# Optimization experiments

Hardware: AMD Instinct MI355X
Metric: run time of the kernel (lower is better)

The kernel has to match this reference:

```python
import jax, jax.numpy as jnp
import numpy as np

B, C, H, W = 8, 256, 64, 64
CK = C // 8  # query/key channels


def setup_inputs() -> dict:
    key = jax.random.key(0)
    ks = jax.random.split(key, 8)
    s = 1.0 / np.sqrt(C)
    return {
        "x": jax.random.normal(ks[0], (B, C, H, W), dtype=jnp.float32),
        "Wq": jax.random.normal(ks[1], (CK, C), dtype=jnp.float32) * s,
        "bq": jax.random.normal(ks[2], (CK,), dtype=jnp.float32) * 0.01,
        "Wk": jax.random.normal(ks[3], (CK, C), dtype=jnp.float32) * s,
        "bk": jax.random.normal(ks[4], (CK,), dtype=jnp.float32) * 0.01,
        "Wv": jax.random.normal(ks[5], (C, C), dtype=jnp.float32) * s,
        "bv": jax.random.normal(ks[6], (C,), dtype=jnp.float32) * 0.01,
        "gamma": jax.random.normal(ks[7], (1,), dtype=jnp.float32) * 0.1,
    }


def reference(x, Wq, bq, Wk, bk, Wv, bv, gamma):
    b, c, h, w = x.shape
    n = h * w
    xf = x.reshape(b, c, n)                       # [B,C,N]
    # 1x1 convs == channel-wise linear maps
    q = jnp.einsum('oc,bcn->bon', Wq, xf) + bq[:, None]   # [B,CK,N]
    k = jnp.einsum('oc,bcn->bon', Wk, xf) + bk[:, None]   # [B,CK,N]
    v = jnp.einsum('oc,bcn->bon', Wv, xf) + bv[:, None]   # [B,C,N]
    energy = jnp.einsum('bcm,bcn->bmn', q, k)             # [B,N,N] (query rows m)
    attn = jax.nn.softmax(energy, axis=-1)
    out = jnp.einsum('bcn,bmn->bcm', v, attn)             # value @ attn^T
    out = out.reshape(b, c, h, w)
    return gamma * out + x
```

## Files before the change

### kernel.cpp

```cpp
#include <hip/hip_runtime.h>
#include <stdint.h>

typedef unsigned short u16;
typedef __bf16 bf16_t;
typedef __bf16 bf16x4 __attribute__((ext_vector_type(4)));
typedef __bf16 bf16x8 __attribute__((ext_vector_type(8)));
typedef float f32x4 __attribute__((ext_vector_type(4)));

#define LOG2E 1.4426950408889634f

__device__ __forceinline__ u16 f2bf(float f) {
    union { float f; unsigned int u; } v; v.f = f;
    unsigned int r = v.u + 0x7fffu + ((v.u >> 16) & 1u);
    return (u16)(r >> 16);
}

__device__ __forceinline__ bf16x8 ld8f_bf(const float* __restrict__ p) {
    float4 a = *reinterpret_cast<const float4*>(p);
    float4 b = *reinterpret_cast<const float4*>(p + 4);
    bf16x8 r;
    r[0] = (bf16_t)a.x; r[1] = (bf16_t)a.y; r[2] = (bf16_t)a.z; r[3] = (bf16_t)a.w;
    r[4] = (bf16_t)b.x; r[5] = (bf16_t)b.y; r[6] = (bf16_t)b.z; r[7] = (bf16_t)b.w;
    return r;
}

__global__ __launch_bounds__(256) void k_transpose(const float* __restrict__ x,
                                                   u16* __restrict__ xT) {
    __shared__ u16 tile[64][68];
    int blk = blockIdx.x;
    int b = blk >> 8;
    int r = blk & 255;
    int c0 = (r & 3) * 64;
    int n0 = (r >> 2) * 64;
    const float* xb = x + (size_t)b * 256 * 4096;
    u16* xTb = xT + (size_t)b * 4096 * 256;
    int t = threadIdx.x;
    int lc = t >> 4;
    int l4 = (t & 15) * 4;
    #pragma unroll
    for (int p = 0; p < 4; ++p) {
        int c = lc + p * 16;
        float4 v = *reinterpret_cast<const float4*>(xb + (size_t)(c0 + c) * 4096 + n0 + l4);
        tile[c][l4 + 0] = f2bf(v.x); tile[c][l4 + 1] = f2bf(v.y);
        tile[c][l4 + 2] = f2bf(v.z); tile[c][l4 + 3] = f2bf(v.w);
    }
    __syncthreads();
    #pragma unroll
    for (int p = 0; p < 4; ++p) {
        int n = lc + p * 16;
        ushort4 v;
        v.x = tile[l4 + 0][n]; v.y = tile[l4 + 1][n];
        v.z = tile[l4 + 2][n]; v.w = tile[l4 + 3][n];
        *reinterpret_cast<ushort4*>(xTb + (size_t)(n0 + n) * 256 + c0 + l4) = v;
    }
}

__global__ __launch_bounds__(256, 2) void k_proj(
    const u16* __restrict__ xT,
    const float* __restrict__ Wq, const float* __restrict__ bq,
    const float* __restrict__ Wk, const float* __restrict__ bk,
    const float* __restrict__ Wv, const float* __restrict__ bv,
    u16* __restrict__ qt, u16* __restrict__ kt, u16* __restrict__ vn) {
    __shared__ u16 Xs[64 * 256];
    __shared__ u16 Ws[64 * 256];
    __shared__ u16 Wvs[256 * 32];
    int blk = blockIdx.x;
    int b = blk & 7;
    int n0 = (blk >> 3) * 64;
    int t = threadIdx.x;
    int w = t >> 6;
    int lane = t & 63;
    int lo = lane & 15;
    int q = lane >> 4;
    const u16* xTb = xT + (size_t)b * 4096 * 256;

    #pragma unroll
    for (int p = 0; p < 8; ++p) {
        int G = p * 256 + t;
        int n = G >> 5, g = G & 31;
        bf16x8 v = *reinterpret_cast<const bf16x8*>(
            xTb + (size_t)(n0 + n) * 256 + g * 8);
        *reinterpret_cast<bf16x8*>(&Xs[(n * 32 + (g ^ (n & 7))) * 8]) = v;
        const float* src = (n < 32) ? (Wq + (size_t)n * 256 + g * 8)
                                    : (Wk + (size_t)(n - 32) * 256 + g * 8);
        *reinterpret_cast<bf16x8*>(&Ws[(n * 32 + (g ^ (n & 7))) * 8]) = ld8f_bf(src);
    }

    f32x4 accqk[4] = {};
    f32x4 accv[16];
    #pragma unroll
    for (int i = 0; i < 16; ++i) accv[i] = f32x4{0.f, 0.f, 0.f, 0.f};

    int rowA = w * 16 + lo;
    int cw = w * 64;
    for (int c0 = 0; c0 < 256; c0 += 32) {
        __syncthreads();
        #pragma unroll
        for (int p = 0; p < 4; ++p) {
            int G = p * 256 + t;
            int co = G >> 2, g2 = G & 3;
            *reinterpret_cast<bf16x8*>(&Wvs[(co * 4 + (g2 ^ (co & 3))) * 8]) =
                ld8f_bf(Wv + (size_t)co * 256 + c0 + g2 * 8);
        }
        __syncthreads();

        int K = c0 >> 3;
        bf16x8 a = *reinterpret_cast<const bf16x8*>(
            &Xs[(rowA * 32 + ((K + q) ^ (lo & 7))) * 8]);
        #pragma unroll
        for (int ot = 0; ot < 4; ++ot) {
            bf16x8 bb = *reinterpret_cast<const bf16x8*>(
                &Ws[((ot * 16 + lo) * 32 + ((K + q) ^ (lo & 7))) * 8]);
            accqk[ot] = __builtin_amdgcn_mfma_f32_16x16x32_bf16(a, bb, accqk[ot], 0, 0, 0);
        }
        bf16x8 xbf[4];
        #pragma unroll
        for (int nt = 0; nt < 4; ++nt)
            xbf[nt] = *reinterpret_cast<const bf16x8*>(
                &Xs[((nt * 16 + lo) * 32 + ((K + q) ^ (lo & 7))) * 8]);
        #pragma unroll
        for (int ct = 0; ct < 4; ++ct) {
            int co = cw + ct * 16 + lo;
            bf16x8 av = *reinterpret_cast<const bf16x8*>(
                &Wvs[(co * 4 + (q ^ (co & 3))) * 8]);
            #pragma unroll
            for (int nt = 0; nt < 4; ++nt)
                accv[ct * 4 + nt] = __builtin_amdgcn_mfma_f32_16x16x32_bf16(
                    av, xbf[nt], accv[ct * 4 + nt], 0, 0, 0);
        }
    }
    #pragma unroll
    for (int ot = 0; ot < 4; ++ot) {
        float bias = (ot < 2) ? bq[ot * 16 + lo] : bk[(ot - 2) * 16 + lo];
        #pragma unroll
        for (int r = 0; r < 4; ++r) {
            int n = n0 + w * 16 + q * 4 + r;
            float val = accqk[ot][r] + bias;
            if (ot < 2) qt[((size_t)b * 4096 + n) * 32 + ot * 16 + lo] = f2bf(val);
            else        kt[((size_t)b * 4096 + n) * 32 + (ot - 2) * 16 + lo] = f2bf(val);
        }
    }
    #pragma unroll
    for (int ct = 0; ct < 4; ++ct) {
        #pragma unroll
        for (int nt = 0; nt < 4; ++nt) {
            #pragma unroll
            for (int r = 0; r < 4; ++r) {
                int co = cw + ct * 16 + q * 4 + r;
                float val = accv[ct * 4 + nt][r] + bv[co];
                vn[((size_t)b * 256 + co) * 4096 + n0 + nt * 16 + lo] = f2bf(val);
            }
        }
    }
}

__global__ __launch_bounds__(256, 2) void k_flash(
    const u16* __restrict__ qt, const u16* __restrict__ kt,
    const u16* __restrict__ vn, const float* __restrict__ x,
    const float* __restrict__ gamma, float* __restrict__ out) {
    __shared__ bf16_t E_lds[2][128 * 72];
    __shared__ float l_lds[128];
    int blk = blockIdx.x;
    int b = blk & 7;
    int rest = blk >> 3;
    int m0 = (rest & 31) * 128;
    int ch0 = (rest >> 5) * 128;
    int t = threadIdx.x;
    int w = t >> 6;
    int lane = t & 63;
    int lo = lane & 15;
    int q = lane >> 4;
    const u16* qtb = qt + (size_t)b * 4096 * 32;
    const u16* ktb = kt + (size_t)b * 4096 * 32;
    const u16* vb = vn + (size_t)b * 256 * 4096;

    int qw0 = m0 + w * 32;
    int cw0 = ch0 + w * 32;

    bf16x8 qfrag[2];
    #pragma unroll
    for (int qm = 0; qm < 2; ++qm)
        qfrag[qm] = *reinterpret_cast<const bf16x8*>(
            qtb + (size_t)(qw0 + qm * 16 + lo) * 32 + q * 8);

    f32x4 O[2][8];
    #pragma unroll
    for (int ct = 0; ct < 2; ++ct)
        #pragma unroll
        for (int mt = 0; mt < 8; ++mt) O[ct][mt] = f32x4{0.f, 0.f, 0.f, 0.f};
    float lsum[2] = {0.f, 0.f};
    const f32x4 zero = {0.f, 0.f, 0.f, 0.f};

    {
        bf16x8 kf[4];
        #pragma unroll
        for (int nt = 0; nt < 4; ++nt)
            kf[nt] = *reinterpret_cast<const bf16x8*>(
                ktb + (size_t)(nt * 16 + lo) * 32 + q * 8);
        #pragma unroll
        for (int qm = 0; qm < 2; ++qm)
            #pragma unroll
            for (int nt = 0; nt < 4; ++nt) {
                f32x4 St = __builtin_amdgcn_mfma_f32_16x16x32_bf16(
                    kf[nt], qfrag[qm], zero, 0, 0, 0);
                bf16x4 pp;
                #pragma unroll
                for (int r = 0; r < 4; ++r) {
                    float p = __builtin_amdgcn_exp2f(St[r] * LOG2E);
                    lsum[qm] += p;
                    pp[r] = (bf16_t)p;
                }
                *reinterpret_cast<bf16x4*>(
                    &E_lds[0][(qw0 - m0 + qm * 16 + lo) * 72 + nt * 16 + q * 4]) = pp;
            }
    }
    __syncthreads();

    for (int s = 0; s < 64; ++s) {
        int n0 = s * 64;
        const bf16_t* Er = E_lds[s & 1];
        bf16_t* Ew = E_lds[(s + 1) & 1];
        if (s + 1 < 64) {
            bf16x8 kf[4];
            #pragma unroll
            for (int nt = 0; nt < 4; ++nt)
                kf[nt] = *reinterpret_cast<const bf16x8*>(
                    ktb + (size_t)(n0 + 64 + nt * 16 + lo) * 32 + q * 8);
            #pragma unroll
            for (int qm = 0; qm < 2; ++qm)
                #pragma unroll
                for (int nt = 0; nt < 4; ++nt) {
                    f32x4 St = __builtin_amdgcn_mfma_f32_16x16x32_bf16(
                        kf[nt], qfrag[qm], zero, 0, 0, 0);
                    bf16x4 pp;
                    #pragma unroll
                    for (int r = 0; r < 4; ++r) {
                        float p = __builtin_amdgcn_exp2f(St[r] * LOG2E);
                        lsum[qm] += p;
                        pp[r] = (bf16_t)p;
                    }
                    *reinterpret_cast<bf16x4*>(
                        &Ew[(qw0 - m0 + qm * 16 + lo) * 72 + nt * 16 + q * 4]) = pp;
                }
        }
        #pragma unroll
        for (int kk = 0; kk < 2; ++kk) {
            bf16x8 vf[2];
            #pragma unroll
            for (int ct = 0; ct < 2; ++ct)
                vf[ct] = *reinterpret_cast<const bf16x8*>(
                    vb + (size_t)(cw0 + ct * 16 + lo) * 4096 + n0 + kk * 32 + q * 8);
            #pragma unroll
            for (int mt = 0; mt < 8; ++mt) {
                bf16x8 pf = *reinterpret_cast<const bf16x8*>(
                    &Er[(mt * 16 + lo) * 72 + kk * 32 + q * 8]);
                #pragma unroll
                for (int ct = 0; ct < 2; ++ct)
                    O[ct][mt] = __builtin_amdgcn_mfma_f32_16x16x32_bf16(
                        vf[ct], pf, O[ct][mt], 0, 0, 0);
            }
        }
        __syncthreads();
    }

    #pragma unroll
    for (int qm = 0; qm < 2; ++qm) {
        lsum[qm] += __shfl_xor(lsum[qm], 16, 64);
        lsum[qm] += __shfl_xor(lsum[qm], 32, 64);
        if (q == 0) l_lds[qw0 - m0 + qm * 16 + lo] = lsum[qm];
    }
    __syncthreads();

    float g = gamma[0];
    const float* xb = x + (size_t)b * 256 * 4096;
    float* ob = out + (size_t)b * 256 * 4096;
    float linv[8];
    #pragma unroll
    for (int mt = 0; mt < 8; ++mt) linv[mt] = 1.0f / l_lds[mt * 16 + lo];
    #pragma unroll
    for (int ct = 0; ct < 2; ++ct) {
        #pragma unroll
        for (int mt = 0; mt < 8; ++mt) {
            int m = m0 + mt * 16 + lo;
            #pragma unroll
            for (int r = 0; r < 4; ++r) {
                int c = cw0 + ct * 16 + q * 4 + r;
                size_t idx = (size_t)c * 4096 + m;
                ob[idx] = g * (O[ct][mt][r] * linv[mt]) + xb[idx];
            }
        }
    }
}

extern "C" void kernel_launch(void* const* d_in, const int* in_sizes, int n_in,
                              void* d_out, int out_size, void* d_ws, size_t ws_size,
                              hipStream_t stream) {
    const float* x     = (const float*)d_in[0];
    const float* Wq    = (const float*)d_in[1];
    const float* bq    = (const float*)d_in[2];
    const float* Wk    = (const float*)d_in[3];
    const float* bk    = (const float*)d_in[4];
    const float* Wv    = (const float*)d_in[5];
    const float* bv    = (const float*)d_in[6];
    const float* gamma = (const float*)d_in[7];
    float* out = (float*)d_out;

    char* ws = (char*)d_ws;
    u16* xT = (u16*)d_out;
    u16* qt = (u16*)ws;
    u16* kt = (u16*)(ws + 2097152);
    u16* vn = (u16*)(ws + 2 * 2097152);

    k_transpose<<<2048, 256, 0, stream>>>(x, xT);
    k_proj<<<512, 256, 0, stream>>>(xT, Wq, bq, Wk, bk, Wv, bv, qt, kt, vn);
    k_flash<<<512, 256, 0, stream>>>(qt, kt, vn, x, gamma, out);
}
```

Before: 237.9 us.

## Keep softmax probabilities in registers with 32x32 MFMA, dropping LDS staging

Measured after the change: 370.5 us. +55.8%, slower.

```diff
diff --git a/kernel.cpp b/kernel.cpp
--- a/kernel.cpp
+++ b/kernel.cpp
@@ -2,12 +2,15 @@
 #include <stdint.h>
 
 typedef unsigned short u16;
+typedef unsigned int u32;
 typedef __bf16 bf16_t;
 typedef __bf16 bf16x4 __attribute__((ext_vector_type(4)));
 typedef __bf16 bf16x8 __attribute__((ext_vector_type(8)));
 typedef float f32x4 __attribute__((ext_vector_type(4)));
+typedef float f32x16 __attribute__((ext_vector_type(16)));
 
 #define LOG2E 1.4426950408889634f
+#define MFMA32(a, b, c) __builtin_amdgcn_mfma_f32_32x32x16_bf16(a, b, c, 0, 0, 0)
 
 __device__ __forceinline__ u16 f2bf(float f) {
     union { float f; unsigned int u; } v; v.f = f;
@@ -22,6 +25,28 @@
     r[0] = (bf16_t)a.x; r[1] = (bf16_t)a.y; r[2] = (bf16_t)a.z; r[3] = (bf16_t)a.w;
     r[4] = (bf16_t)b.x; r[5] = (bf16_t)b.y; r[6] = (bf16_t)b.z; r[7] = (bf16_t)b.w;
     return r;
+}
+
+__device__ __forceinline__ u32 cvt_pk_bf16(float a, float b) {
+    u32 r;
+    asm("v_cvt_pk_bf16_f32 %0, %1, %2" : "=v"(r) : "v"(a), "v"(b));
+    return r;
+}
+
+__device__ __forceinline__ void plane32_swap(u32& a, u32& b) {
+    asm("v_permlane32_swap_b32 %0, %1" : "+v"(a), "+v"(b));
+}
+
+__device__ __forceinline__ bf16x8 pack8(const float* p) {
+    u32 c0 = cvt_pk_bf16(p[0], p[1]);
+    u32 c1 = cvt_pk_bf16(p[2], p[3]);
+    u32 c2 = cvt_pk_bf16(p[4], p[5]);
+    u32 c3 = cvt_pk_bf16(p[6], p[7]);
+    plane32_swap(c0, c2);
+    plane32_swap(c1, c3);
+    union { u32 u[4]; bf16x8 v; } f;
+    f.u[0] = c0; f.u[1] = c1; f.u[2] = c2; f.u[3] = c3;
+    return f.v;
 }
 
 __global__ __launch_bounds__(256) void k_transpose(const float* __restrict__ x,
@@ -136,7 +161,7 @@
         for (int r = 0; r < 4; ++r) {
             int n = n0 + w * 16 + q * 4 + r;
             float val = accqk[ot][r] + bias;
-            if (ot < 2) qt[((size_t)b * 4096 + n) * 32 + ot * 16 + lo] = f2bf(val);
+            if (ot < 2) qt[((size_t)b * 4096 + n) * 32 + ot * 16 + lo] = f2bf(val * LOG2E);
             else        kt[((size_t)b * 4096 + n) * 32 + (ot - 2) * 16 + lo] = f2bf(val);
         }
     }
@@ -158,8 +183,6 @@
     const u16* __restrict__ qt, const u16* __restrict__ kt,
     const u16* __restrict__ vn, const float* __restrict__ x,
     const float* __restrict__ gamma, float* __restrict__ out) {
-    __shared__ bf16_t E_lds[2][128 * 72];
-    __shared__ float l_lds[128];
     int blk = blockIdx.x;
     int b = blk & 7;
     int rest = blk >> 3;
@@ -168,127 +191,118 @@
     int t = threadIdx.x;
     int w = t >> 6;
     int lane = t & 63;
-    int lo = lane & 15;
-    int q = lane >> 4;
+    int la = lane & 31;
+    int hi = lane >> 5;
+
     const u16* qtb = qt + (size_t)b * 4096 * 32;
     const u16* ktb = kt + (size_t)b * 4096 * 32;
-    const u16* vb = vn + (size_t)b * 256 * 4096;
+    const u16* vbp = vn + (size_t)b * 256 * 4096;
 
     int qw0 = m0 + w * 32;
-    int cw0 = ch0 + w * 32;
-
-    bf16x8 qfrag[2];
-    #pragma unroll
-    for (int qm = 0; qm < 2; ++qm)
-        qfrag[qm] = *reinterpret_cast<const bf16x8*>(
-            qtb + (size_t)(qw0 + qm * 16 + lo) * 32 + q * 8);
-
-    f32x4 O[2][8];
-    #pragma unroll
-    for (int ct = 0; ct < 2; ++ct)
-        #pragma unroll
-        for (int mt = 0; mt < 8; ++mt) O[ct][mt] = f32x4{0.f, 0.f, 0.f, 0.f};
-    float lsum[2] = {0.f, 0.f};
-    const f32x4 zero = {0.f, 0.f, 0.f, 0.f};
-
-    {
-        bf16x8 kf[4];
-        #pragma unroll
-        for (int nt = 0; nt < 4; ++nt)
-            kf[nt] = *reinterpret_cast<const bf16x8*>(
-                ktb + (size_t)(nt * 16 + lo) * 32 + q * 8);
-        #pragma unroll
-        for (int qm = 0; qm < 2; ++qm)
-            #pragma unroll
-            for (int nt = 0; nt < 4; ++nt) {
-                f32x4 St = __builtin_amdgcn_mfma_f32_16x16x32_bf16(
-                    kf[nt], qfrag[qm], zero, 0, 0, 0);
-                bf16x4 pp;
-                #pragma unroll
-                for (int r = 0; r < 4; ++r) {
-                    float p = __builtin_amdgcn_exp2f(St[r] * LOG2E);
-                    lsum[qm] += p;
-                    pp[r] = (bf16_t)p;
-                }
-                *reinterpret_cast<bf16x4*>(
-                    &E_lds[0][(qw0 - m0 + qm * 16 + lo) * 72 + nt * 16 + q * 4]) = pp;
-            }
-    }
-    __syncthreads();
+    bf16x8 qf0 = *reinterpret_cast<const bf16x8*>(qtb + (size_t)(qw0 + la) * 32 + hi * 8);
+    bf16x8 qf1 = *reinterpret_cast<const bf16x8*>(qtb + (size_t)(qw0 + la) * 32 + 16 + hi * 8);
+
+    f32x16 O0 = {}, O1 = {}, O2 = {}, O3 = {};
+    const f32x16 z16 = {};
+    float lsum = 0.f;
+
+    const u16* kp  = ktb + (size_t)la * 32 + hi * 8;
+    const u16* vp0 = vbp + (size_t)(ch0 +  0 + la) * 4096 + hi * 8;
+    const u16* vp1 = vbp + (size_t)(ch0 + 32 + la) * 4096 + hi * 8;
+    const u16* vp2 = vbp + (size_t)(ch0 + 64 + la) * 4096 + hi * 8;
+    const u16* vp3 = vbp + (size_t)(ch0 + 96 + la) * 4096 + hi * 8;
+
+    bf16x8 kf0 = *reinterpret_cast<const bf16x8*>(kp);
+    bf16x8 kf1 = *reinterpret_cast<const bf16x8*>(kp + 16);
+    bf16x8 kf2 = *reinterpret_cast<const bf16x8*>(kp + 1024);
+    bf16x8 kf3 = *reinterpret_cast<const bf16x8*>(kp + 1040);
 
     for (int s = 0; s < 64; ++s) {
         int n0 = s * 64;
-        const bf16_t* Er = E_lds[s & 1];
-        bf16_t* Ew = E_lds[(s + 1) & 1];
-        if (s + 1 < 64) {
-            bf16x8 kf[4];
-            #pragma unroll
-            for (int nt = 0; nt < 4; ++nt)
-                kf[nt] = *reinterpret_cast<const bf16x8*>(
-                    ktb + (size_t)(n0 + 64 + nt * 16 + lo) * 32 + q * 8);
-            #pragma unroll
-            for (int qm = 0; qm < 2; ++qm)
-                #pragma unroll
-                for (int nt = 0; nt < 4; ++nt) {
-                    f32x4 St = __builtin_amdgcn_mfma_f32_16x16x32_bf16(
-                        kf[nt], qfrag[qm], zero, 0, 0, 0);
-                    bf16x4 pp;
-                    #pragma unroll
-                    for (int r = 0; r < 4; ++r) {
-                        float p = __builtin_amdgcn_exp2f(St[r] * LOG2E);
-                        lsum[qm] += p;
-                        pp[r] = (bf16_t)p;
-                    }
-                    *reinterpret_cast<bf16x4*>(
-                        &Ew[(qw0 - m0 + qm * 16 + lo) * 72 + nt * 16 + q * 4]) = pp;
-                }
-        }
-        #pragma unroll
-        for (int kk = 0; kk < 2; ++kk) {
-            bf16x8 vf[2];
-            #pragma unroll
-            for (int ct = 0; ct < 2; ++ct)
-                vf[ct] = *reinterpret_cast<const bf16x8*>(
-                    vb + (size_t)(cw0 + ct * 16 + lo) * 4096 + n0 + kk * 32 + q * 8);
-            #pragma unroll
-            for (int mt = 0; mt < 8; ++mt) {
-                bf16x8 pf = *reinterpret_cast<const bf16x8*>(
-                    &Er[(mt * 16 + lo) * 72 + kk * 32 + q * 8]);
-                #pragma unroll
-                for (int ct = 0; ct < 2; ++ct)
-                    O[ct][mt] = __builtin_amdgcn_mfma_f32_16x16x32_bf16(
-                        vf[ct], pf, O[ct][mt], 0, 0, 0);
-            }
-        }
-        __syncthreads();
-    }
-
-    #pragma unroll
-    for (int qm = 0; qm < 2; ++qm) {
-        lsum[qm] += __shfl_xor(lsum[qm], 16, 64);
-        lsum[qm] += __shfl_xor(lsum[qm], 32, 64);
-        if (q == 0) l_lds[qw0 - m0 + qm * 16 + lo] = lsum[qm];
-    }
-    __syncthreads();
-
+        int nn = (s < 63) ? (n0 + 64) : 0;
+        const u16* kpn = kp + (size_t)nn * 32;
+        bf16x8 kn0 = *reinterpret_cast<const bf16x8*>(kpn);
+        bf16x8 kn1 = *reinterpret_cast<const bf16x8*>(kpn + 16);
+        bf16x8 kn2 = *reinterpret_cast<const bf16x8*>(kpn + 1024);
+        bf16x8 kn3 = *reinterpret_cast<const bf16x8*>(kpn + 1040);
+
+        f32x16 S0 = MFMA32(kf0, qf0, z16);
+        S0 = MFMA32(kf1, qf1, S0);
+
+        bf16x8 va0 = *reinterpret_cast<const bf16x8*>(vp0 + n0);
+        bf16x8 va1 = *reinterpret_cast<const bf16x8*>(vp1 + n0);
+        bf16x8 va2 = *reinterpret_cast<const bf16x8*>(vp2 + n0);
+        bf16x8 va3 = *reinterpret_cast<const bf16x8*>(vp3 + n0);
+        bf16x8 vb0 = *reinterpret_cast<const bf16x8*>(vp0 + n0 + 16);
+        bf16x8 vb1 = *reinterpret_cast<const bf16x8*>(vp1 + n0 + 16);
+        bf16x8 vb2 = *reinterpret_cast<const bf16x8*>(vp2 + n0 + 16);
+        bf16x8 vb3 = *reinterpret_cast<const bf16x8*>(vp3 + n0 + 16);
+
+        f32x16 S1 = MFMA32(kf2, qf0, z16);
+        S1 = MFMA32(kf3, qf1, S1);
+
+        float p0[16];
+        #pragma unroll
+        for (int i = 0; i < 16; ++i) {
+            p0[i] = __builtin_amdgcn_exp2f(S0[i]);
+            lsum += p0[i];
+        }
+        bf16x8 fA = pack8(p0);
+        bf16x8 fB = pack8(p0 + 8);
+
+        bf16x8 vc0 = *reinterpret_cast<const bf16x8*>(vp0 + n0 + 32);
+        bf16x8 vc1 = *reinterpret_cast<const bf16x8*>(vp1 + n0 + 32);
+        bf16x8 vc2 = *reinterpret_cast<const bf16x8*>(vp2 + n0 + 32);
+        bf16x8 vc3 = *reinterpret_cast<const bf16x8*>(vp3 + n0 + 32);
+        bf16x8 vd0 = *reinterpret_cast<const bf16x8*>(vp0 + n0 + 48);
+        bf16x8 vd1 = *reinterpret_cast<const bf16x8*>(vp1 + n0 + 48);
+        bf16x8 vd2 = *reinterpret_cast<const bf16x8*>(vp2 + n0 + 48);
+        bf16x8 vd3 = *reinterpret_cast<const bf16x8*>(vp3 + n0 + 48);
+
+        O0 = MFMA32(va0, fA, O0);
+        O1 = MFMA32(va1, fA, O1);
+        O2 = MFMA32(va2, fA, O2);
+        O3 = MFMA32(va3, fA, O3);
+        O0 = MFMA32(vb0, fB, O0);
+        O1 = MFMA32(vb1, fB, O1);
+        O2 = MFMA32(vb2, fB, O2);
+        O3 = MFMA32(vb3, fB, O3);
+
+        float p1[16];
+        #pragma unroll
+        for (int i = 0; i < 16; ++i) {
+            p1[i] = __builtin_amdgcn_exp2f(S1[i]);
+            lsum += p1[i];
+        }
+        bf16x8 fC = pack8(p1);
+        bf16x8 fD = pack8(p1 + 8);
+
+        O0 = MFMA32(vc0, fC, O0);
+        O1 = MFMA32(vc1, fC, O1);
+        O2 = MFMA32(vc2, fC, O2);
+        O3 = MFMA32(vc3, fC, O3);
+        O0 = MFMA32(vd0, fD, O0);
+        O1 = MFMA32(vd1, fD, O1);
+        O2 = MFMA32(vd2, fD, O2);
+        O3 = MFMA32(vd3, fD, O3);
+
+        kf0 = kn0; kf1 = kn1; kf2 = kn2; kf3 = kn3;
+    }
+
+    lsum += __shfl_xor(lsum, 32, 64);
+    float linv = 1.0f / lsum;
     float g = gamma[0];
     const float* xb = x + (size_t)b * 256 * 4096;
     float* ob = out + (size_t)b * 256 * 4096;
-    float linv[8];
-    #pragma unroll
-    for (int mt = 0; mt < 8; ++mt) linv[mt] = 1.0f / l_lds[mt * 16 + lo];
-    #pragma unroll
-    for (int ct = 0; ct < 2; ++ct) {
-        #pragma unroll
-        for (int mt = 0; mt < 8; ++mt) {
-            int m = m0 + mt * 16 + lo;
-            #pragma unroll
-            for (int r = 0; r < 4; ++r) {
-                int c = cw0 + ct * 16 + q * 4 + r;
-                size_t idx = (size_t)c * 4096 + m;
-                ob[idx] = g * (O[ct][mt][r] * linv[mt]) + xb[idx];
-            }
-        }
+    int m = m0 + w * 32 + la;
+    #pragma unroll
+    for (int r = 0; r < 16; ++r) {
+        int crow = (r & 3) + 8 * (r >> 2) + 4 * hi;
+        size_t i0 = (size_t)(ch0 + crow) * 4096 + m;
+        ob[i0]             = g * (O0[r] * linv) + xb[i0];
+        ob[i0 + 32 * 4096] = g * (O1[r] * linv) + xb[i0 + 32 * 4096];
+        ob[i0 + 64 * 4096] = g * (O2[r] * linv) + xb[i0 + 64 * 4096];
+        ob[i0 + 96 * 4096] = g * (O3[r] * linv) + xb[i0 + 96 * 4096];
     }
 }
 
```
